# Optimization experiments

Measured on AMD Instinct MI355X. Metric: run time of the kernel, lower is better.

The kernel has to match this reference:

```python
import jax, jax.numpy as jnp
import numpy as np


def _pairwise_dist(pred, target):
    # pred: [B, N, 3], target: [B, M, 3] -> [B, N, M]
    p2 = jnp.sum(pred * pred, axis=-1, keepdims=True)          # [B, N, 1]
    t2 = jnp.sum(target * target, axis=-1)[:, None, :]          # [B, 1, M]
    cross = jnp.einsum('bnd,bmd->bnm', pred, target)            # [B, N, M]
    sq = jnp.maximum(p2 + t2 - 2.0 * cross, 0.0)
    return jnp.sqrt(sq)


def setup_inputs() -> dict:
    key = jax.random.key(0)
    k1, k2 = jax.random.split(key)
    pred = jax.random.normal(k1, (2, 16384, 3), dtype=jnp.float32)
    target = jax.random.normal(k2, (2, 16384, 3), dtype=jnp.float32)
    return {"pred": pred, "target": target}


def reference(pred, target):
    d = _pairwise_dist(pred, target)            # [B, N, M]
    forward_min = jnp.min(d, axis=2)            # [B, N] nearest target per pred point
    backward_min = jnp.min(d, axis=1)           # [B, M] nearest pred per target point
    return jnp.mean(forward_min) + jnp.mean(backward_min)
```

## Files before the change

### kernel.cpp

```cpp
#include <hip/hip_runtime.h>
#include <math.h>

#define NPTS 16384
#define NB   2
#define RCH  1024
#define NRC  (NPTS / RCH)
#define TILES (RCH / 32)
#define QPB  256
#define NQC  (NPTS / QPB)
#define TOTQ (NB * NPTS)
#define TOTMIN (2 * TOTQ)

typedef short bf16x8 __attribute__((ext_vector_type(8)));

__device__ __forceinline__ unsigned ordf(float f) {
    unsigned b = __float_as_uint(f);
    return (b & 0x80000000u) ? ~b : (b | 0x80000000u);
}
__device__ __forceinline__ float deordf(unsigned u) {
    return __uint_as_float((u & 0x80000000u) ? (u ^ 0x80000000u) : ~u);
}
__device__ __forceinline__ unsigned short bfr(float v) {
    unsigned u = __float_as_uint(v);
    u += 0x7FFFu + ((u >> 16) & 1u);
    return (unsigned short)(u >> 16);
}
__device__ __forceinline__ float ubf(unsigned short h) {
    return __uint_as_float(((unsigned)h) << 16);
}

#define TILE_STEP(ac, B0, B1, mA0, mB0, mA1, mB1)                          \
    asm("v_mfma_f32_32x32x16_bf16 v[32:47], %4, %5, 0\n\t"                 \
        "v_mfma_f32_32x32x16_bf16 v[48:63], %4, %6, 0\n\t"                 \
        "s_nop 7\n\t"                                                      \
        "s_nop 6\n\t"                                                      \
        "v_min3_f32 %0, %0, v32, v33\n\t"                                  \
        "v_min3_f32 %1, %1, v34, v35\n\t"                                  \
        "v_min3_f32 %0, %0, v36, v37\n\t"                                  \
        "v_min3_f32 %1, %1, v38, v39\n\t"                                  \
        "v_min3_f32 %0, %0, v40, v41\n\t"                                  \
        "v_min3_f32 %1, %1, v42, v43\n\t"                                  \
        "v_min3_f32 %0, %0, v44, v45\n\t"                                  \
        "v_min3_f32 %1, %1, v46, v47\n\t"                                  \
        "v_min3_f32 %2, %2, v48, v49\n\t"                                  \
        "v_min3_f32 %3, %3, v50, v51\n\t"                                  \
        "v_min3_f32 %2, %2, v52, v53\n\t"                                  \
        "v_min3_f32 %3, %3, v54, v55\n\t"                                  \
        "v_min3_f32 %2, %2, v56, v57\n\t"                                  \
        "v_min3_f32 %3, %3, v58, v59\n\t"                                  \
        "v_min3_f32 %2, %2, v60, v61\n\t"                                  \
        "v_min3_f32 %3, %3, v62, v63\n\t"                                  \
        : "+v"(mA0), "+v"(mB0), "+v"(mA1), "+v"(mB1)                       \
        : "v"(ac), "v"(B0), "v"(B1)                                        \
        : "v32","v33","v34","v35","v36","v37","v38","v39",                 \
          "v40","v41","v42","v43","v44","v45","v46","v47",                 \
          "v48","v49","v50","v51","v52","v53","v54","v55",                 \
          "v56","v57","v58","v59","v60","v61","v62","v63")

__global__ __launch_bounds__(256) void prep_kernel(const float* __restrict__ pred,
                                                   const float* __restrict__ target,
                                                   unsigned short* __restrict__ panel,
                                                   unsigned short* __restrict__ qpack,
                                                   float* __restrict__ wq,
                                                   unsigned* __restrict__ mins) {
    int t = blockIdx.x * 256 + threadIdx.x;
    int cloud = t >> 15, r = t & 32767, b = r >> 14, i = r & 16383;
    const float* src = cloud ? target : pred;
    float x = src[(b * NPTS + i) * 3 + 0];
    float y = src[(b * NPTS + i) * 3 + 1];
    float zz = src[(b * NPTS + i) * 3 + 2];
    float w = 0.5f * (x * x + y * y + zz * zz);

    unsigned short hx = bfr(x),  lx = bfr(x - ubf(hx));
    unsigned short hy = bfr(y),  ly = bfr(y - ubf(hy));
    unsigned short hz = bfr(zz), lz = bfr(zz - ubf(hz));
    unsigned short hw = bfr(w),  lw = bfr(w - ubf(hw));

    const int slot = cloud * 2 + b;

    unsigned short* pp = panel + ((size_t)slot << 18) + (size_t)(i >> 5) * 512 + (size_t)(i & 31) * 8;
    uint4 k0, k1;
    k0.x = hx | ((unsigned)lx << 16);
    k0.y = hx | ((unsigned)hy << 16);
    k0.z = ly | ((unsigned)hy << 16);
    k0.w = hz | ((unsigned)lz << 16);
    *(uint4*)pp = k0;
    k1.x = hz | ((unsigned)hw << 16);
    k1.y = lw;
    k1.z = 0; k1.w = 0;
    *(uint4*)(pp + 256) = k1;

    const unsigned short S = 0x8000u, ONE = 0x3F80u;
    unsigned short nhx = hx ^ S, nlx = lx ^ S, nhy = hy ^ S, nly = ly ^ S, nhz = hz ^ S, nlz = lz ^ S;
    unsigned short* qp = qpack + ((size_t)slot << 18) + (size_t)i * 16;
    uint4 qlo, qhi;
    qlo.x = nhx | ((unsigned)nhx << 16);
    qlo.y = nlx | ((unsigned)nhy << 16);
    qlo.z = nhy | ((unsigned)nly << 16);
    qlo.w = nhz | ((unsigned)nhz << 16);
    qhi.x = nlz | ((unsigned)ONE << 16);
    qhi.y = ONE;
    qhi.z = 0; qhi.w = 0;
    *(uint4*)qp = qlo;
    *(uint4*)(qp + 8) = qhi;

    wq[(slot << 14) | i] = w;
    mins[(slot << 14) | i] = 0xFFFFFFFFu;
}

__global__ __launch_bounds__(256, 4) void nn_min_kernel(const unsigned short* __restrict__ panel,
                                                        const unsigned short* __restrict__ qpack,
                                                        unsigned* __restrict__ mins) {
    __shared__ __attribute__((aligned(16))) unsigned short lds_s[RCH * 16];

    const int z = blockIdx.z, b = z & 1, qc = z >> 1, rc = 1 - qc;
    const int tid = threadIdx.x, ln = tid & 63, wv = tid >> 6;

    const unsigned short* pbase = panel + (((size_t)(rc * 2 + b)) << 18) + (size_t)blockIdx.x * (RCH * 16);
    uint4 st0 = *(const uint4*)(pbase + (0 * 256 + tid) * 8);
    uint4 st1 = *(const uint4*)(pbase + (1 * 256 + tid) * 8);
    uint4 st2 = *(const uint4*)(pbase + (2 * 256 + tid) * 8);
    uint4 st3 = *(const uint4*)(pbase + (3 * 256 + tid) * 8);
    uint4 st4 = *(const uint4*)(pbase + (4 * 256 + tid) * 8);
    uint4 st5 = *(const uint4*)(pbase + (5 * 256 + tid) * 8);
    uint4 st6 = *(const uint4*)(pbase + (6 * 256 + tid) * 8);
    uint4 st7 = *(const uint4*)(pbase + (7 * 256 + tid) * 8);

    const int qbase = blockIdx.y * QPB;
    const unsigned short* qb = qpack + (((size_t)(qc * 2 + b)) << 18);
    const int qcol = ln & 31, khalf = (ln >> 5) * 8;
    bf16x8 B0 = *(const bf16x8*)(qb + (size_t)(qbase + (wv * 2 + 0) * 32 + qcol) * 16 + khalf);
    bf16x8 B1 = *(const bf16x8*)(qb + (size_t)(qbase + (wv * 2 + 1) * 32 + qcol) * 16 + khalf);

    *(uint4*)&lds_s[(0 * 256 + tid) * 8] = st0;
    *(uint4*)&lds_s[(1 * 256 + tid) * 8] = st1;
    *(uint4*)&lds_s[(2 * 256 + tid) * 8] = st2;
    *(uint4*)&lds_s[(3 * 256 + tid) * 8] = st3;
    *(uint4*)&lds_s[(4 * 256 + tid) * 8] = st4;
    *(uint4*)&lds_s[(5 * 256 + tid) * 8] = st5;
    *(uint4*)&lds_s[(6 * 256 + tid) * 8] = st6;
    *(uint4*)&lds_s[(7 * 256 + tid) * 8] = st7;
    __syncthreads();

    float mA0 = INFINITY, mB0 = INFINITY, mA1 = INFINITY, mB1 = INFINITY;

    bf16x8 a0 = *(const bf16x8*)&lds_s[0 * 512 + ln * 8];
    bf16x8 a1 = *(const bf16x8*)&lds_s[1 * 512 + ln * 8];

    #pragma unroll
    for (int t = 0; t < TILES; t += 2) {
        bf16x8 n0, n1;
        if (t + 2 < TILES) {
            n0 = *(const bf16x8*)&lds_s[(t + 2) * 512 + ln * 8];
            n1 = *(const bf16x8*)&lds_s[(t + 3) * 512 + ln * 8];
        }
        TILE_STEP(a0, B0, B1, mA0, mB0, mA1, mB1);
        TILE_STEP(a1, B0, B1, mA0, mB0, mA1, mB1);
        a0 = n0; a1 = n1;
    }

    unsigned* om = mins + ((size_t)z << 14) + qbase;
    atomicMin(&om[(wv * 2 + 0) * 32 + qcol], ordf(fminf(mA0, mB0)));
    atomicMin(&om[(wv * 2 + 1) * 32 + qcol], ordf(fminf(mA1, mB1)));
}

__global__ __launch_bounds__(256) void reduceA_kernel(const unsigned* __restrict__ mins,
                                                      const float* __restrict__ wq,
                                                      float* __restrict__ partials) {
    int base = blockIdx.x * 1024;
    float s = 0.f;
    #pragma unroll
    for (int k = 0; k < 4; ++k) {
        int t = base + k * 256 + threadIdx.x;
        float m = deordf(mins[t]);
        s += sqrtf(fmaxf(0.f, 2.f * (wq[t] + m)));
    }
    #pragma unroll
    for (int off = 32; off; off >>= 1) s += __shfl_down(s, off);
    __shared__ float wsum[4];
    int lane = threadIdx.x & 63, wv = threadIdx.x >> 6;
    if (lane == 0) wsum[wv] = s;
    __syncthreads();
    if (threadIdx.x == 0) partials[blockIdx.x] = wsum[0] + wsum[1] + wsum[2] + wsum[3];
}

__global__ void reduceB_kernel(const float* __restrict__ partials, float* __restrict__ out) {
    float s = partials[threadIdx.x];
    #pragma unroll
    for (int off = 32; off; off >>= 1) s += __shfl_down(s, off);
    if (threadIdx.x == 0) out[0] = s / (float)TOTQ;
}

extern "C" void kernel_launch(void* const* d_in, const int* in_sizes, int n_in,
                              void* d_out, int out_size, void* d_ws, size_t ws_size,
                              hipStream_t stream) {
    const float* pred   = (const float*)d_in[0];
    const float* target = (const float*)d_in[1];
    char* ws = (char*)d_ws;

    unsigned short* panel = (unsigned short*)ws;
    unsigned short* qpack = (unsigned short*)(ws + (size_t)2 * 1024 * 1024);
    float*          wq    = (float*)(ws + (size_t)4 * 1024 * 1024);
    unsigned*       mins  = (unsigned*)(ws + (size_t)4 * 1024 * 1024 + 256 * 1024);
    float*       partials = (float*)(ws + (size_t)4 * 1024 * 1024 + 512 * 1024);
    float* out = (float*)d_out;

    prep_kernel<<<TOTMIN / 256, 256, 0, stream>>>(pred, target, panel, qpack, wq, mins);

    dim3 grid(NRC, NQC, 2 * NB);
    nn_min_kernel<<<grid, 256, 0, stream>>>(panel, qpack, mins);

    reduceA_kernel<<<64, 256, 0, stream>>>(mins, wq, partials);
    reduceB_kernel<<<1, 64, 0, stream>>>(partials, out);
}
```

Before: 44.39 us.

## Stream 8192-point reference panels through double-buffered direct-to-LDS loads

Each block now processes 8192 reference points instead of 1024, staging 1024-point chunks into a double-buffered LDS area with global_load_lds, so the load of the next chunk overlaps the MFMA min computation on the current one. This cuts the grid size by a factor of eight and reduces the number of atomicMin operations per query. The cost is 64KB of LDS per block and the loss of the occupancy hint, which lowers occupancy and leaves fewer blocks to fill the GPU's compute units.

```diff
diff --git a/kernel.cpp b/kernel.cpp
--- a/kernel.cpp
+++ b/kernel.cpp
@@ -3,9 +3,10 @@
 
 #define NPTS 16384
 #define NB   2
-#define RCH  1024
-#define NRC  (NPTS / RCH)
-#define TILES (RCH / 32)
+#define RPB  8192
+#define NRC  (NPTS / RPB)
+#define NCH  8
+#define CHREF 1024
 #define QPB  256
 #define NQC  (NPTS / QPB)
 #define TOTQ (NB * NPTS)
@@ -28,6 +29,10 @@
 __device__ __forceinline__ float ubf(unsigned short h) {
     return __uint_as_float(((unsigned)h) << 16);
 }
+
+#define GLD16(gp, lp) __builtin_amdgcn_global_load_lds(                         \
+    (const __attribute__((address_space(1))) unsigned int*)(gp),                \
+    (__attribute__((address_space(3))) unsigned int*)(lp), 16, 0, 0)
 
 #define TILE_STEP(ac, B0, B1, mA0, mB0, mA1, mB1)                          \
     asm("v_mfma_f32_32x32x16_bf16 v[32:47], %4, %5, 0\n\t"                 \
@@ -108,23 +113,16 @@
     mins[(slot << 14) | i] = 0xFFFFFFFFu;
 }
 
-__global__ __launch_bounds__(256, 4) void nn_min_kernel(const unsigned short* __restrict__ panel,
-                                                        const unsigned short* __restrict__ qpack,
-                                                        unsigned* __restrict__ mins) {
-    __shared__ __attribute__((aligned(16))) unsigned short lds_s[RCH * 16];
+__global__ __launch_bounds__(256) void nn_min_kernel(const unsigned short* __restrict__ panel,
+                                                     const unsigned short* __restrict__ qpack,
+                                                     unsigned* __restrict__ mins) {
+    __shared__ __attribute__((aligned(16))) unsigned short lds_s[2 * 16384];
 
     const int z = blockIdx.z, b = z & 1, qc = z >> 1, rc = 1 - qc;
     const int tid = threadIdx.x, ln = tid & 63, wv = tid >> 6;
 
-    const unsigned short* pbase = panel + (((size_t)(rc * 2 + b)) << 18) + (size_t)blockIdx.x * (RCH * 16);
-    uint4 st0 = *(const uint4*)(pbase + (0 * 256 + tid) * 8);
-    uint4 st1 = *(const uint4*)(pbase + (1 * 256 + tid) * 8);
-    uint4 st2 = *(const uint4*)(pbase + (2 * 256 + tid) * 8);
-    uint4 st3 = *(const uint4*)(pbase + (3 * 256 + tid) * 8);
-    uint4 st4 = *(const uint4*)(pbase + (4 * 256 + tid) * 8);
-    uint4 st5 = *(const uint4*)(pbase + (5 * 256 + tid) * 8);
-    uint4 st6 = *(const uint4*)(pbase + (6 * 256 + tid) * 8);
-    uint4 st7 = *(const uint4*)(pbase + (7 * 256 + tid) * 8);
+    const char* pblock = (const char*)(panel + (((size_t)(rc * 2 + b)) << 18)
+                                       + (size_t)blockIdx.x * (RPB * 16));
 
     const int qbase = blockIdx.y * QPB;
     const unsigned short* qb = qpack + (((size_t)(qc * 2 + b)) << 18);
@@ -132,32 +130,46 @@
     bf16x8 B0 = *(const bf16x8*)(qb + (size_t)(qbase + (wv * 2 + 0) * 32 + qcol) * 16 + khalf);
     bf16x8 B1 = *(const bf16x8*)(qb + (size_t)(qbase + (wv * 2 + 1) * 32 + qcol) * 16 + khalf);
 
-    *(uint4*)&lds_s[(0 * 256 + tid) * 8] = st0;
-    *(uint4*)&lds_s[(1 * 256 + tid) * 8] = st1;
-    *(uint4*)&lds_s[(2 * 256 + tid) * 8] = st2;
-    *(uint4*)&lds_s[(3 * 256 + tid) * 8] = st3;
-    *(uint4*)&lds_s[(4 * 256 + tid) * 8] = st4;
-    *(uint4*)&lds_s[(5 * 256 + tid) * 8] = st5;
-    *(uint4*)&lds_s[(6 * 256 + tid) * 8] = st6;
-    *(uint4*)&lds_s[(7 * 256 + tid) * 8] = st7;
+    float mA0 = INFINITY, mB0 = INFINITY, mA1 = INFINITY, mB1 = INFINITY;
+
+#define STAGE(c, h) do {                                                        \
+        const char* g_ = pblock + (size_t)(c) * 32768 + wv * 1024 + ln * 16;    \
+        char* l_ = (char*)lds_s + (h) * 32768 + wv * 1024;                      \
+        _Pragma("unroll")                                                       \
+        for (int r_ = 0; r_ < 8; ++r_)                                          \
+            GLD16(g_ + r_ * 4096, l_ + r_ * 4096);                              \
+    } while (0)
+
+#define COMPUTE(h) do {                                                         \
+        const unsigned short* buf_ = lds_s + (h) * 16384;                       \
+        bf16x8 a0 = *(const bf16x8*)&buf_[0 * 512 + ln * 8];                    \
+        bf16x8 a1 = *(const bf16x8*)&buf_[1 * 512 + ln * 8];                    \
+        _Pragma("unroll")                                                       \
+        for (int t_ = 0; t_ < 32; t_ += 2) {                                    \
+            bf16x8 n0 = a0, n1 = a1;                                            \
+            if (t_ + 2 < 32) {                                                  \
+                n0 = *(const bf16x8*)&buf_[(t_ + 2) * 512 + ln * 8];            \
+                n1 = *(const bf16x8*)&buf_[(t_ + 3) * 512 + ln * 8];            \
+            }                                                                   \
+            TILE_STEP(a0, B0, B1, mA0, mB0, mA1, mB1);                          \
+            TILE_STEP(a1, B0, B1, mA0, mB0, mA1, mB1);                          \
+            a0 = n0; a1 = n1;                                                   \
+        }                                                                       \
+    } while (0)
+
+    STAGE(0, 0);
+    asm volatile("s_waitcnt vmcnt(0)" ::: "memory");
     __syncthreads();
 
-    float mA0 = INFINITY, mB0 = INFINITY, mA1 = INFINITY, mB1 = INFINITY;
-
-    bf16x8 a0 = *(const bf16x8*)&lds_s[0 * 512 + ln * 8];
-    bf16x8 a1 = *(const bf16x8*)&lds_s[1 * 512 + ln * 8];
-
-    #pragma unroll
-    for (int t = 0; t < TILES; t += 2) {
-        bf16x8 n0, n1;
-        if (t + 2 < TILES) {
-            n0 = *(const bf16x8*)&lds_s[(t + 2) * 512 + ln * 8];
-            n1 = *(const bf16x8*)&lds_s[(t + 3) * 512 + ln * 8];
-        }
-        TILE_STEP(a0, B0, B1, mA0, mB0, mA1, mB1);
-        TILE_STEP(a1, B0, B1, mA0, mB0, mA1, mB1);
-        a0 = n0; a1 = n1;
+    #pragma unroll
+    for (int c = 0; c < NCH; ++c) {
+        if (c + 1 < NCH) STAGE(c + 1, (c + 1) & 1);
+        COMPUTE(c & 1);
+        asm volatile("s_waitcnt vmcnt(0)" ::: "memory");
+        __syncthreads();
     }
+#undef STAGE
+#undef COMPUTE
 
     unsigned* om = mins + ((size_t)z << 14) + qbase;
     atomicMin(&om[(wv * 2 + 0) * 32 + qcol], ordf(fminf(mA0, mB0)));
```

Result: no change. 45.14 us (+1.7%).
